# Kernel tuning notes

Measured on AMD Instinct MI355X. Metric: run time of the kernel, lower is better.

The kernel has to match this reference:

```python
import jax, jax.numpy as jnp
import numpy as np
from jax import lax

B, L, H, K = 64, 1024, 768, 4
C1, C2 = 0.1, 0.1


def crf_marginals(feats, maskf, T):
    """Batched linear-chain CRF forward-backward.
    feats: [B,L,K] emission scores, maskf: [B,L] float (1=valid), T: [K,K] transitions.
    Returns marginals [B,L,K] (zeroed at padded positions)."""
    a0 = feats[:, 0]  # [B,K]

    def fwd_step(a, xs):
        f_t, m_t = xs  # [B,K], [B]
        new = f_t + jax.nn.logsumexp(a[:, :, None] + T[None], axis=1)
        a = jnp.where(m_t[:, None] > 0, new, a)  # freeze alpha past last valid token
        return a, a

    _, alphas_rest = lax.scan(fwd_step, a0,
                              (jnp.swapaxes(feats[:, 1:], 0, 1), maskf[:, 1:].T))
    alphas = jnp.concatenate([a0[None], alphas_rest], axis=0)  # [L,B,K]
    logZ = jax.nn.logsumexp(alphas[-1], axis=-1)  # [B] (alpha frozen at last valid t)

    bL = jnp.zeros_like(a0)

    def bwd_step(b, xs):
        f_n, m_n = xs  # emission/mask at t+1
        new = jax.nn.logsumexp(T[None] + (f_n + b)[:, None, :], axis=2)
        b = jnp.where(m_n[:, None] > 0, new, b)  # beta stays 0 until last valid token
        return b, b

    xs = (jnp.swapaxes(feats[:, 1:][:, ::-1], 0, 1), maskf[:, 1:][:, ::-1].T)
    _, betas_rev = lax.scan(bwd_step, bL, xs)
    betas = jnp.concatenate([bL[None], betas_rev], axis=0)[::-1]  # [L,B,K]

    marg = jnp.exp(alphas + betas - logZ[None, :, None]) * maskf.T[:, :, None]
    return jnp.swapaxes(marg, 0, 1)  # [B,L,K]


def _forward(hidden, maskf, w, b, T):
    feats = hidden @ w.T + b                      # [B,L,K] feat2tri
    marg = crf_marginals(feats, maskf, T)
    sp = marg[:, :, 1]                            # select_polarities, masked [B,L]
    gamma = sp.sum(axis=1) / 2.0                  # [B]
    sent_vs = jnp.einsum('bl,blh->bh', sp, hidden) / gamma[:, None]
    s_prob = sp / gamma[:, None]                  # padded-ragged per-token probs
    s_prob_norm = jnp.abs(s_prob).sum(axis=1).mean()
    pena = jax.nn.relu(T[1, 0] - T[0, 0]) + jax.nn.relu(T[0, 1] - T[1, 1])
    norm_pen = C1 * pena + C2 * s_prob_norm
    return sent_vs, norm_pen, s_prob


def setup_inputs():
    key = jax.random.key(0)
    ks = jax.random.split(key, 8)
    hidden = jax.random.normal(ks[0], (B, L, H), dtype=jnp.float32)
    seq_lens = jax.random.randint(ks[1], (B,), L // 4, L + 1)
    # hidden_mask: 0 for valid tokens, nonzero for padding (forward uses mask = hidden_mask==0)
    hidden_mask = (jnp.arange(L)[None, :] >= seq_lens[:, None]).astype(jnp.int32)
    subj_position = jax.random.randint(ks[2], (B, L), -20, 21)
    obj_position = jax.random.randint(ks[3], (B, L), -20, 21)
    pe_inputs = jax.random.randint(ks[4], (B, L), 0, 2 * L)
    pe_binary = jax.random.randint(ks[5], (B, L), 0, 2)
    w_feat2tri = jax.random.normal(ks[6], (K, H), dtype=jnp.float32) * (1.0 / np.sqrt(H)).astype(np.float32)
    b_feat2tri = jnp.zeros((K,), dtype=jnp.float32)
    transitions = jax.random.normal(ks[7], (K, K), dtype=jnp.float32) * 0.1
    return dict(hidden=hidden, hidden_mask=hidden_mask, subj_position=subj_position,
                obj_position=obj_position, seq_lens=seq_lens, pe_inputs=pe_inputs,
                pe_binary=pe_binary, w_feat2tri=w_feat2tri, b_feat2tri=b_feat2tri,
                transitions=transitions)


def reference(hidden, hidden_mask, subj_position, obj_position, seq_lens, pe_inputs,
              pe_binary, w_feat2tri, b_feat2tri, transitions):
    maskf = (hidden_mask == 0).astype(hidden.dtype)
    # relevance is computed in the original forward but never consumed downstream,
    # so it has no effect on outputs; omitted here.
    return _forward(hidden, maskf, w_feat2tri, b_feat2tri, transitions)
```

## Files before the change

### kernel.cpp

```cpp
#include <hip/hip_runtime.h>

#define B 64
#define L 1024
#define H 768
#define NROWS (B * L)
#define LOG2E 1.4426950408889634f
#define CS 16
#define NCH 64
#define NEG -1e30f

#define EXP2(x) __builtin_amdgcn_exp2f(x)
#define LOG2(x) __builtin_amdgcn_logf(x)

__global__ __launch_bounds__(256) void feats_kernel(
    const float* __restrict__ hidden, const float* __restrict__ w,
    const float* __restrict__ bias, float4* __restrict__ featsT)
{
    const int lane = threadIdx.x & 63;
    const int wave = (blockIdx.x * blockDim.x + threadIdx.x) >> 6;
    const int nwaves = (gridDim.x * blockDim.x) >> 6;

    float wr[3][4][4];
#pragma unroll
    for (int c = 0; c < 3; ++c)
#pragma unroll
        for (int j = 0; j < 4; ++j)
#pragma unroll
            for (int k = 0; k < 4; ++k)
                wr[c][j][k] = w[k * H + lane * 4 + 256 * c + j];
    const float bb0 = bias[0], bb1 = bias[1], bb2 = bias[2], bb3 = bias[3];

    for (int row = wave; row < NROWS; row += nwaves) {
        const float4* hrow = reinterpret_cast<const float4*>(hidden) + (size_t)row * (H / 4);
        float acc[4] = {0.f, 0.f, 0.f, 0.f};
#pragma unroll
        for (int c = 0; c < 3; ++c) {
            float4 h = hrow[lane + 64 * c];
            const float hv[4] = {h.x, h.y, h.z, h.w};
#pragma unroll
            for (int j = 0; j < 4; ++j)
#pragma unroll
                for (int k = 0; k < 4; ++k)
                    acc[k] = fmaf(hv[j], wr[c][j][k], acc[k]);
        }
#pragma unroll
        for (int k = 0; k < 4; ++k) {
            float v = acc[k];
#pragma unroll
            for (int s = 32; s >= 1; s >>= 1) v += __shfl_xor(v, s, 64);
            acc[k] = v;
        }
        if (lane == 0) {
            const int b = row >> 10, l = row & 1023;
            featsT[l * B + b] = make_float4((acc[0] + bb0) * LOG2E, (acc[1] + bb1) * LOG2E,
                                            (acc[2] + bb2) * LOG2E, (acc[3] + bb3) * LOG2E);
        }
    }
}

__global__ __launch_bounds__(64) void chunkmat_kernel(
    const float4* __restrict__ featsT, const int* __restrict__ seq_lens,
    const float* __restrict__ T, float* __restrict__ mats)
{
    const int b = threadIdx.x;
    const int dir = blockIdx.x >= NCH;
    const int c = blockIdx.x - (dir ? NCH : 0);
    const int sl = seq_lens[b];
    const int lo = c * CS + 1;
    const int hi = min(c * CS + CS, L - 1);
    const int ns = hi - lo + 1;

    float eT2[4][4];
#pragma unroll
    for (int i = 0; i < 4; ++i)
#pragma unroll
        for (int j = 0; j < 4; ++j) eT2[i][j] = EXP2(T[i * 4 + j] * LOG2E);

    float4 fr[CS];
#pragma unroll
    for (int u = 0; u < CS; ++u) {
        const int t = dir ? max(hi - u, lo) : min(lo + u, hi);
        fr[u] = featsT[t * B + b];
    }

    float M[4][4];
#pragma unroll
    for (int i = 0; i < 4; ++i)
#pragma unroll
        for (int j = 0; j < 4; ++j) M[i][j] = (i == j) ? 0.f : NEG;

    if (dir == 0) {
#pragma unroll
        for (int u = 0; u < CS; ++u) {
            const int t = lo + u;
            const bool valid = (u < ns) && (t < sl);
            const float f[4] = {fr[u].x, fr[u].y, fr[u].z, fr[u].w};
            float nM[4][4];
#pragma unroll
            for (int i = 0; i < 4; ++i) {
                const float rm = fmaxf(fmaxf(M[i][0], M[i][1]), fmaxf(M[i][2], M[i][3]));
                const float e0 = EXP2(M[i][0] - rm), e1 = EXP2(M[i][1] - rm);
                const float e2 = EXP2(M[i][2] - rm), e3 = EXP2(M[i][3] - rm);
#pragma unroll
                for (int j = 0; j < 4; ++j) {
                    const float s = (e0 * eT2[0][j] + e1 * eT2[1][j]) + (e2 * eT2[2][j] + e3 * eT2[3][j]);
                    nM[i][j] = f[j] + rm + LOG2(s);
                }
            }
#pragma unroll
            for (int i = 0; i < 4; ++i)
#pragma unroll
                for (int j = 0; j < 4; ++j) M[i][j] = valid ? nM[i][j] : M[i][j];
        }
    } else {
#pragma unroll
        for (int u = 0; u < CS; ++u) {
            const int n = hi - u;
            const bool valid = (u < ns) && (n < sl);
            const float f[4] = {fr[u].x, fr[u].y, fr[u].z, fr[u].w};
            float nM[4][4];
#pragma unroll
            for (int j = 0; j < 4; ++j) {
                const float c0 = f[0] + M[0][j], c1 = f[1] + M[1][j];
                const float c2 = f[2] + M[2][j], c3 = f[3] + M[3][j];
                const float cm = fmaxf(fmaxf(c0, c1), fmaxf(c2, c3));
                const float g0 = EXP2(c0 - cm), g1 = EXP2(c1 - cm);
                const float g2 = EXP2(c2 - cm), g3 = EXP2(c3 - cm);
#pragma unroll
                for (int i = 0; i < 4; ++i) {
                    const float s = (g0 * eT2[i][0] + g1 * eT2[i][1]) + (g2 * eT2[i][2] + g3 * eT2[i][3]);
                    nM[i][j] = cm + LOG2(s);
                }
            }
#pragma unroll
            for (int i = 0; i < 4; ++i)
#pragma unroll
                for (int j = 0; j < 4; ++j) M[i][j] = valid ? nM[i][j] : M[i][j];
        }
    }
#pragma unroll
    for (int i = 0; i < 4; ++i)
#pragma unroll
        for (int j = 0; j < 4; ++j)
            mats[((dir * NCH + c) * 16 + i * 4 + j) * B + b] = M[i][j];
}

__global__ __launch_bounds__(128) void bound_kernel(
    const float4* __restrict__ featsT, const float* __restrict__ mats,
    float* __restrict__ vbound, float* __restrict__ alpha1,
    float* __restrict__ beta1, float* __restrict__ logZ)
{
    const int b = threadIdx.x & 63;
    const int dir = threadIdx.x >> 6;

    float Ms[4][16];
#pragma unroll
    for (int p = 0; p < 3; ++p) {
        const int cc = dir ? (NCH - 1 - p) : p;
#pragma unroll
        for (int k = 0; k < 16; ++k)
            Ms[p][k] = mats[((dir * NCH + cc) * 16 + k) * B + b];
    }

    float v0, v1, v2, v3;
    if (dir == 0) {
        const float4 f0 = featsT[b];
        v0 = f0.x; v1 = f0.y; v2 = f0.z; v3 = f0.w;
        alpha1[b] = v1;
    } else {
        v0 = v1 = v2 = v3 = 0.f;
        beta1[(L - 1) * B + b] = 0.f;
    }

#pragma unroll
    for (int u = 0; u < NCH; ++u) {
        const int cc = dir ? (NCH - 1 - u) : u;
        vbound[((dir * NCH + cc) * 4 + 0) * B + b] = v0;
        vbound[((dir * NCH + cc) * 4 + 1) * B + b] = v1;
        vbound[((dir * NCH + cc) * 4 + 2) * B + b] = v2;
        vbound[((dir * NCH + cc) * 4 + 3) * B + b] = v3;
        if (u + 3 < NCH) {
            const int cp = dir ? (NCH - 1 - (u + 3)) : (u + 3);
#pragma unroll
            for (int k = 0; k < 16; ++k)
                Ms[(u + 3) & 3][k] = mats[((dir * NCH + cp) * 16 + k) * B + b];
        }
        float n[4];
        if (dir == 0) {
#pragma unroll
            for (int j = 0; j < 4; ++j) {
                const float c0 = v0 + Ms[u & 3][0 * 4 + j], c1 = v1 + Ms[u & 3][1 * 4 + j];
                const float c2 = v2 + Ms[u & 3][2 * 4 + j], c3 = v3 + Ms[u & 3][3 * 4 + j];
                const float m = fmaxf(fmaxf(c0, c1), fmaxf(c2, c3));
                const float s = (EXP2(c0 - m) + EXP2(c1 - m)) + (EXP2(c2 - m) + EXP2(c3 - m));
                n[j] = m + LOG2(s);
            }
        } else {
#pragma unroll
            for (int i = 0; i < 4; ++i) {
                const float c0 = v0 + Ms[u & 3][i * 4 + 0], c1 = v1 + Ms[u & 3][i * 4 + 1];
                const float c2 = v2 + Ms[u & 3][i * 4 + 2], c3 = v3 + Ms[u & 3][i * 4 + 3];
                const float m = fmaxf(fmaxf(c0, c1), fmaxf(c2, c3));
                const float s = (EXP2(c0 - m) + EXP2(c1 - m)) + (EXP2(c2 - m) + EXP2(c3 - m));
                n[i] = m + LOG2(s);
            }
        }
        v0 = n[0]; v1 = n[1]; v2 = n[2]; v3 = n[3];
    }
    if (dir == 0) {
        const float m = fmaxf(fmaxf(v0, v1), fmaxf(v2, v3));
        logZ[b] = m + LOG2(EXP2(v0 - m) + EXP2(v1 - m) + EXP2(v2 - m) + EXP2(v3 - m));
    }
}

__global__ __launch_bounds__(64) void rescan_kernel(
    const float4* __restrict__ featsT, const int* __restrict__ seq_lens,
    const float* __restrict__ T, const float* __restrict__ vbound,
    float* __restrict__ alpha1, float* __restrict__ beta1)
{
    const int b = threadIdx.x;
    const int dir = blockIdx.x >= NCH;
    const int c = blockIdx.x - (dir ? NCH : 0);
    const int sl = seq_lens[b];
    const int lo = c * CS + 1;
    const int hi = min(c * CS + CS, L - 1);
    const int ns = hi - lo + 1;

    float eT2[4][4];
#pragma unroll
    for (int i = 0; i < 4; ++i)
#pragma unroll
        for (int j = 0; j < 4; ++j) eT2[i][j] = EXP2(T[i * 4 + j] * LOG2E);

    float4 fr[CS];
#pragma unroll
    for (int u = 0; u < CS; ++u) {
        const int t = dir ? max(hi - u, lo) : min(lo + u, hi);
        fr[u] = featsT[t * B + b];
    }

    float v0 = vbound[((dir * NCH + c) * 4 + 0) * B + b];
    float v1 = vbound[((dir * NCH + c) * 4 + 1) * B + b];
    float v2 = vbound[((dir * NCH + c) * 4 + 2) * B + b];
    float v3 = vbound[((dir * NCH + c) * 4 + 3) * B + b];

    if (dir == 0) {
#pragma unroll
        for (int u = 0; u < CS; ++u) {
            if (u < ns) {
                const int t = lo + u;
                const bool valid = t < sl;
                const float4 f = fr[u];
                const float m = fmaxf(fmaxf(v0, v1), fmaxf(v2, v3));
                const float e0 = EXP2(v0 - m), e1 = EXP2(v1 - m), e2 = EXP2(v2 - m), e3 = EXP2(v3 - m);
                const float s0 = (e0 * eT2[0][0] + e1 * eT2[1][0]) + (e2 * eT2[2][0] + e3 * eT2[3][0]);
                const float s1 = (e0 * eT2[0][1] + e1 * eT2[1][1]) + (e2 * eT2[2][1] + e3 * eT2[3][1]);
                const float s2 = (e0 * eT2[0][2] + e1 * eT2[1][2]) + (e2 * eT2[2][2] + e3 * eT2[3][2]);
                const float s3 = (e0 * eT2[0][3] + e1 * eT2[1][3]) + (e2 * eT2[2][3] + e3 * eT2[3][3]);
                const float n0 = f.x + m + LOG2(s0), n1 = f.y + m + LOG2(s1);
                const float n2 = f.z + m + LOG2(s2), n3 = f.w + m + LOG2(s3);
                v0 = valid ? n0 : v0; v1 = valid ? n1 : v1;
                v2 = valid ? n2 : v2; v3 = valid ? n3 : v3;
                alpha1[t * B + b] = v1;
            }
        }
    } else {
#pragma unroll
        for (int u = 0; u < CS; ++u) {
            if (u < ns) {
                const int n = hi - u;
                const bool valid = n < sl;
                const float4 f = fr[u];
                const float c0 = f.x + v0, c1 = f.y + v1, c2 = f.z + v2, c3 = f.w + v3;
                const float m = fmaxf(fmaxf(c0, c1), fmaxf(c2, c3));
                const float g0 = EXP2(c0 - m), g1 = EXP2(c1 - m), g2 = EXP2(c2 - m), g3 = EXP2(c3 - m);
                const float s0 = (g0 * eT2[0][0] + g1 * eT2[0][1]) + (g2 * eT2[0][2] + g3 * eT2[0][3]);
                const float s1 = (g0 * eT2[1][0] + g1 * eT2[1][1]) + (g2 * eT2[1][2] + g3 * eT2[1][3]);
                const float s2 = (g0 * eT2[2][0] + g1 * eT2[2][1]) + (g2 * eT2[2][2] + g3 * eT2[2][3]);
                const float s3 = (g0 * eT2[3][0] + g1 * eT2[3][1]) + (g2 * eT2[3][2] + g3 * eT2[3][3]);
                const float n0 = m + LOG2(s0), n1 = m + LOG2(s1);
                const float n2 = m + LOG2(s2), n3 = m + LOG2(s3);
                v0 = valid ? n0 : v0; v1 = valid ? n1 : v1;
                v2 = valid ? n2 : v2; v3 = valid ? n3 : v3;
                beta1[(n - 1) * B + b] = v1;
            }
        }
    }
}

__global__ __launch_bounds__(256) void marg_kernel(
    const float* __restrict__ alpha1, const float* __restrict__ beta1,
    const float* __restrict__ logZ, const int* __restrict__ seq_lens,
    float* __restrict__ normsum, float* __restrict__ sprob)
{
    const int b = blockIdx.x;
    const int tid = threadIdx.x;
    const float lz = logZ[b];
    const int sl = seq_lens[b];
    float v[4];
    float loc = 0.f;
#pragma unroll
    for (int c = 0; c < 4; ++c) {
        const int l = tid + 256 * c;
        const float a1 = alpha1[l * B + b];
        const float be = beta1[l * B + b];
        const float x = (l < sl) ? EXP2(a1 + be - lz) : 0.f;
        v[c] = x;
        loc += x;
    }
#pragma unroll
    for (int s = 32; s >= 1; s >>= 1) loc += __shfl_xor(loc, s, 64);
    __shared__ float red[4];
    if ((tid & 63) == 0) red[tid >> 6] = loc;
    __syncthreads();
    const float tot = red[0] + red[1] + red[2] + red[3];
    const float g = 0.5f * tot;
    const float inv = 1.0f / g;
#pragma unroll
    for (int c = 0; c < 4; ++c)
        sprob[b * L + tid + 256 * c] = v[c] * inv;
    if (tid == 0) normsum[b] = tot * inv;
}

__global__ __launch_bounds__(256) void sentv_kernel(
    const float* __restrict__ hidden, const float* __restrict__ sprob,
    float* __restrict__ partial)
{
    const int b = blockIdx.y;
    const int hc = blockIdx.x % 3;
    const int lc = blockIdx.x / 3;
    const int h = hc * 256 + threadIdx.x;
    const float* hb = hidden + ((size_t)b * L + (size_t)lc * 256) * H + h;
    const float* sp = sprob + b * L + lc * 256;
    float acc = 0.f;
#pragma unroll 8
    for (int l = 0; l < 256; ++l)
        acc = fmaf(sp[l], hb[(size_t)l * H], acc);
    partial[((size_t)lc * B + b) * H + h] = acc;
}

__global__ __launch_bounds__(256) void final_kernel(
    const float* __restrict__ partial, const float* __restrict__ normsum,
    const float* __restrict__ T, float* __restrict__ out)
{
    const int idx = blockIdx.x * 256 + threadIdx.x;
    if (idx < B * H) {
        out[idx] = (partial[idx] + partial[B * H + idx]) +
                   (partial[2 * B * H + idx] + partial[3 * B * H + idx]);
    }
    if (idx == 0) {
        const float pena = fmaxf(T[4] - T[0], 0.f) + fmaxf(T[1] - T[5], 0.f);
        float s = 0.f;
        for (int b2 = 0; b2 < B; ++b2) s += normsum[b2];
        out[B * H] = 0.1f * pena + 0.1f * (s / 64.f);
    }
}

extern "C" void kernel_launch(void* const* d_in, const int* in_sizes, int n_in,
                              void* d_out, int out_size, void* d_ws, size_t ws_size,
                              hipStream_t stream) {
    const float* hidden   = (const float*)d_in[0];
    const int*   seq_lens = (const int*)d_in[4];
    const float* w        = (const float*)d_in[7];
    const float* bias     = (const float*)d_in[8];
    const float* T        = (const float*)d_in[9];

    float* ws = (float*)d_ws;
    float4* featsT  = (float4*)(ws);
    float*  alpha1  = ws + 262144;
    float*  beta1   = ws + 327680;
    float*  logZ    = ws + 393216;
    float*  normsum = ws + 393280;
    float*  partial = ws + 393344;
    float*  mats    = ws + 589952;
    float*  vbound  = ws + 721024;

    float* out   = (float*)d_out;
    float* sprob = out + B * H + 1;

    feats_kernel<<<2048, 256, 0, stream>>>(hidden, w, bias, featsT);
    chunkmat_kernel<<<2 * NCH, 64, 0, stream>>>(featsT, seq_lens, T, mats);
    bound_kernel<<<1, 128, 0, stream>>>(featsT, mats, vbound, alpha1, beta1, logZ);
    rescan_kernel<<<2 * NCH, 64, 0, stream>>>(featsT, seq_lens, T, vbound, alpha1, beta1);
    marg_kernel<<<64, 256, 0, stream>>>(alpha1, beta1, logZ, seq_lens, normsum, sprob);
    sentv_kernel<<<dim3(12, 64), 256, 0, stream>>>(hidden, sprob, partial);
    final_kernel<<<192, 256, 0, stream>>>(partial, normsum, T, out);
}
```

Baseline: 103.8 us.

## Fuse rescan with marginals via shared memory and vectorize sentv over hidden dim

```diff
diff --git a/kernel.cpp b/kernel.cpp
--- a/kernel.cpp
+++ b/kernel.cpp
@@ -58,13 +58,13 @@
     }
 }
 
-__global__ __launch_bounds__(64) void chunkmat_kernel(
+__global__ __launch_bounds__(128) void chunkmat_kernel(
     const float4* __restrict__ featsT, const int* __restrict__ seq_lens,
     const float* __restrict__ T, float* __restrict__ mats)
 {
-    const int b = threadIdx.x;
-    const int dir = blockIdx.x >= NCH;
-    const int c = blockIdx.x - (dir ? NCH : 0);
+    const int b = threadIdx.x & 63;
+    const int dir = threadIdx.x >> 6;
+    const int c = blockIdx.x;
     const int sl = seq_lens[b];
     const int lo = c * CS + 1;
     const int hi = min(c * CS + CS, L - 1);
@@ -147,8 +147,7 @@
 
 __global__ __launch_bounds__(128) void bound_kernel(
     const float4* __restrict__ featsT, const float* __restrict__ mats,
-    float* __restrict__ vbound, float* __restrict__ alpha1,
-    float* __restrict__ beta1, float* __restrict__ logZ)
+    float* __restrict__ vbound, float* __restrict__ logZ)
 {
     const int b = threadIdx.x & 63;
     const int dir = threadIdx.x >> 6;
@@ -166,10 +165,8 @@
     if (dir == 0) {
         const float4 f0 = featsT[b];
         v0 = f0.x; v1 = f0.y; v2 = f0.z; v3 = f0.w;
-        alpha1[b] = v1;
     } else {
         v0 = v1 = v2 = v3 = 0.f;
-        beta1[(L - 1) * B + b] = 0.f;
     }
 
 #pragma unroll
@@ -213,18 +210,18 @@
     }
 }
 
-__global__ __launch_bounds__(64) void rescan_kernel(
+__global__ __launch_bounds__(128) void rescan_sp_kernel(
     const float4* __restrict__ featsT, const int* __restrict__ seq_lens,
     const float* __restrict__ T, const float* __restrict__ vbound,
-    float* __restrict__ alpha1, float* __restrict__ beta1)
-{
-    const int b = threadIdx.x;
-    const int dir = blockIdx.x >= NCH;
-    const int c = blockIdx.x - (dir ? NCH : 0);
+    const float* __restrict__ logZ, float* __restrict__ spu,
+    float* __restrict__ chunksum)
+{
+    const int tid = threadIdx.x;
+    const int b = tid & 63;
+    const int dir = tid >> 6;
+    const int c = blockIdx.x;
     const int sl = seq_lens[b];
-    const int lo = c * CS + 1;
-    const int hi = min(c * CS + CS, L - 1);
-    const int ns = hi - lo + 1;
+    const int base = c * CS;
 
     float eT2[4][4];
 #pragma unroll
@@ -232,43 +229,24 @@
 #pragma unroll
         for (int j = 0; j < 4; ++j) eT2[i][j] = EXP2(T[i * 4 + j] * LOG2E);
 
-    float4 fr[CS];
-#pragma unroll
-    for (int u = 0; u < CS; ++u) {
-        const int t = dir ? max(hi - u, lo) : min(lo + u, hi);
-        fr[u] = featsT[t * B + b];
-    }
-
-    float v0 = vbound[((dir * NCH + c) * 4 + 0) * B + b];
-    float v1 = vbound[((dir * NCH + c) * 4 + 1) * B + b];
-    float v2 = vbound[((dir * NCH + c) * 4 + 2) * B + b];
-    float v3 = vbound[((dir * NCH + c) * 4 + 3) * B + b];
-
-    if (dir == 0) {
+    __shared__ float ldb[CS * 64];
+
+    if (dir == 1) {
+        float v0 = vbound[((NCH + c) * 4 + 0) * B + b];
+        float v1 = vbound[((NCH + c) * 4 + 1) * B + b];
+        float v2 = vbound[((NCH + c) * 4 + 2) * B + b];
+        float v3 = vbound[((NCH + c) * 4 + 3) * B + b];
+        const bool last = (c == NCH - 1);
+        const int hi_n = last ? (L - 1) : (base + CS);
+        const int cnt = last ? (CS - 1) : CS;
+        if (last) ldb[15 * 64 + b] = v1;
+        float4 fr[CS];
+#pragma unroll
+        for (int u = 0; u < CS; ++u) fr[u] = featsT[max(hi_n - u, base + 1) * B + b];
 #pragma unroll
         for (int u = 0; u < CS; ++u) {
-            if (u < ns) {
-                const int t = lo + u;
-                const bool valid = t < sl;
-                const float4 f = fr[u];
-                const float m = fmaxf(fmaxf(v0, v1), fmaxf(v2, v3));
-                const float e0 = EXP2(v0 - m), e1 = EXP2(v1 - m), e2 = EXP2(v2 - m), e3 = EXP2(v3 - m);
-                const float s0 = (e0 * eT2[0][0] + e1 * eT2[1][0]) + (e2 * eT2[2][0] + e3 * eT2[3][0]);
-                const float s1 = (e0 * eT2[0][1] + e1 * eT2[1][1]) + (e2 * eT2[2][1] + e3 * eT2[3][1]);
-                const float s2 = (e0 * eT2[0][2] + e1 * eT2[1][2]) + (e2 * eT2[2][2] + e3 * eT2[3][2]);
-                const float s3 = (e0 * eT2[0][3] + e1 * eT2[1][3]) + (e2 * eT2[2][3] + e3 * eT2[3][3]);
-                const float n0 = f.x + m + LOG2(s0), n1 = f.y + m + LOG2(s1);
-                const float n2 = f.z + m + LOG2(s2), n3 = f.w + m + LOG2(s3);
-                v0 = valid ? n0 : v0; v1 = valid ? n1 : v1;
-                v2 = valid ? n2 : v2; v3 = valid ? n3 : v3;
-                alpha1[t * B + b] = v1;
-            }
-        }
-    } else {
-#pragma unroll
-        for (int u = 0; u < CS; ++u) {
-            if (u < ns) {
-                const int n = hi - u;
+            if (u < cnt) {
+                const int n = hi_n - u;
                 const bool valid = n < sl;
                 const float4 f = fr[u];
                 const float c0 = f.x + v0, c1 = f.y + v1, c2 = f.z + v2, c3 = f.w + v3;
@@ -282,61 +260,123 @@
                 const float n2 = m + LOG2(s2), n3 = m + LOG2(s3);
                 v0 = valid ? n0 : v0; v1 = valid ? n1 : v1;
                 v2 = valid ? n2 : v2; v3 = valid ? n3 : v3;
-                beta1[(n - 1) * B + b] = v1;
+                ldb[(n - 1 - base) * 64 + b] = v1;
             }
         }
     }
-}
-
-__global__ __launch_bounds__(256) void marg_kernel(
-    const float* __restrict__ alpha1, const float* __restrict__ beta1,
-    const float* __restrict__ logZ, const int* __restrict__ seq_lens,
-    float* __restrict__ normsum, float* __restrict__ sprob)
+
+    float av[CS];
+    if (dir == 0) {
+        float a0 = vbound[(c * 4 + 0) * B + b];
+        float a1 = vbound[(c * 4 + 1) * B + b];
+        float a2 = vbound[(c * 4 + 2) * B + b];
+        float a3 = vbound[(c * 4 + 3) * B + b];
+        av[0] = a1;
+        float4 fr[CS - 1];
+#pragma unroll
+        for (int u = 1; u < CS; ++u) fr[u - 1] = featsT[(base + u) * B + b];
+#pragma unroll
+        for (int u = 1; u < CS; ++u) {
+            const int t = base + u;
+            const bool valid = t < sl;
+            const float4 f = fr[u - 1];
+            const float m = fmaxf(fmaxf(a0, a1), fmaxf(a2, a3));
+            const float e0 = EXP2(a0 - m), e1 = EXP2(a1 - m), e2 = EXP2(a2 - m), e3 = EXP2(a3 - m);
+            const float s0 = (e0 * eT2[0][0] + e1 * eT2[1][0]) + (e2 * eT2[2][0] + e3 * eT2[3][0]);
+            const float s1 = (e0 * eT2[0][1] + e1 * eT2[1][1]) + (e2 * eT2[2][1] + e3 * eT2[3][1]);
+            const float s2 = (e0 * eT2[0][2] + e1 * eT2[1][2]) + (e2 * eT2[2][2] + e3 * eT2[3][2]);
+            const float s3 = (e0 * eT2[0][3] + e1 * eT2[1][3]) + (e2 * eT2[2][3] + e3 * eT2[3][3]);
+            const float n0 = f.x + m + LOG2(s0), n1 = f.y + m + LOG2(s1);
+            const float n2 = f.z + m + LOG2(s2), n3 = f.w + m + LOG2(s3);
+            a0 = valid ? n0 : a0; a1 = valid ? n1 : a1;
+            a2 = valid ? n2 : a2; a3 = valid ? n3 : a3;
+            av[u] = a1;
+        }
+    }
+
+    __syncthreads();
+
+    if (dir == 0) {
+        const float lz = logZ[b];
+        float sp[CS];
+        float local = 0.f;
+#pragma unroll
+        for (int u = 0; u < CS; ++u) {
+            const int l = base + u;
+            const float x = (l < sl) ? EXP2(av[u] + ldb[u * 64 + b] - lz) : 0.f;
+            sp[u] = x;
+            local += x;
+        }
+        float4* dst = reinterpret_cast<float4*>(spu + b * L + base);
+#pragma unroll
+        for (int q = 0; q < 4; ++q)
+            dst[q] = make_float4(sp[4 * q], sp[4 * q + 1], sp[4 * q + 2], sp[4 * q + 3]);
+        chunksum[c * 64 + b] = local;
+    }
+}
+
+__global__ __launch_bounds__(192) void sentv_kernel(
+    const float* __restrict__ hidden, const float* __restrict__ spu,
+    const float* __restrict__ chunksum, float* __restrict__ partial)
+{
+    const int lc = blockIdx.x;
+    const int b = blockIdx.y;
+    const int tid = threadIdx.x;
+
+    __shared__ float s_inv;
+    if (tid < 64) {
+        float v = chunksum[tid * 64 + b];
+#pragma unroll
+        for (int s = 32; s >= 1; s >>= 1) v += __shfl_xor(v, s, 64);
+        if (tid == 0) s_inv = 2.0f / v;
+    }
+    __syncthreads();
+    const float inv = s_inv;
+
+    const float4* hb = reinterpret_cast<const float4*>(hidden + ((size_t)b * L + lc * 256) * H) + tid;
+    const float* sp = spu + b * L + lc * 256;
+
+    float4 acc = make_float4(0.f, 0.f, 0.f, 0.f);
+#pragma unroll 4
+    for (int l0 = 0; l0 < 256; l0 += 4) {
+        const float4 s4 = *reinterpret_cast<const float4*>(sp + l0);
+        const float4 h0 = hb[(size_t)(l0 + 0) * 192];
+        const float4 h1 = hb[(size_t)(l0 + 1) * 192];
+        const float4 h2 = hb[(size_t)(l0 + 2) * 192];
+        const float4 h3 = hb[(size_t)(l0 + 3) * 192];
+        acc.x = fmaf(s4.x, h0.x, acc.x); acc.y = fmaf(s4.x, h0.y, acc.y);
+        acc.z = fmaf(s4.x, h0.z, acc.z); acc.w = fmaf(s4.x, h0.w, acc.w);
+        acc.x = fmaf(s4.y, h1.x, acc.x); acc.y = fmaf(s4.y, h1.y, acc.y);
+        acc.z = fmaf(s4.y, h1.z, acc.z); acc.w = fmaf(s4.y, h1.w, acc.w);
+        acc.x = fmaf(s4.z, h2.x, acc.x); acc.y = fmaf(s4.z, h2.y, acc.y);
+        acc.z = fmaf(s4.z, h2.z, acc.z); acc.w = fmaf(s4.z, h2.w, acc.w);
+        acc.x = fmaf(s4.w, h3.x, acc.x); acc.y = fmaf(s4.w, h3.y, acc.y);
+        acc.z = fmaf(s4.w, h3.z, acc.z); acc.w = fmaf(s4.w, h3.w, acc.w);
+    }
+    acc.x *= inv; acc.y *= inv; acc.z *= inv; acc.w *= inv;
+    reinterpret_cast<float4*>(partial)[((size_t)lc * B + b) * 192 + tid] = acc;
+}
+
+__global__ __launch_bounds__(256) void normalize_kernel(
+    const float* __restrict__ spu, const float* __restrict__ chunksum,
+    float* __restrict__ sprob, float* __restrict__ normsum)
 {
     const int b = blockIdx.x;
     const int tid = threadIdx.x;
-    const float lz = logZ[b];
-    const int sl = seq_lens[b];
-    float v[4];
-    float loc = 0.f;
-#pragma unroll
-    for (int c = 0; c < 4; ++c) {
-        const int l = tid + 256 * c;
-        const float a1 = alpha1[l * B + b];
-        const float be = beta1[l * B + b];
-        const float x = (l < sl) ? EXP2(a1 + be - lz) : 0.f;
-        v[c] = x;
-        loc += x;
-    }
-#pragma unroll
-    for (int s = 32; s >= 1; s >>= 1) loc += __shfl_xor(loc, s, 64);
-    __shared__ float red[4];
-    if ((tid & 63) == 0) red[tid >> 6] = loc;
+    __shared__ float s_tot;
+    if (tid < 64) {
+        float v = chunksum[tid * 64 + b];
+#pragma unroll
+        for (int s = 32; s >= 1; s >>= 1) v += __shfl_xor(v, s, 64);
+        if (tid == 0) s_tot = v;
+    }
     __syncthreads();
-    const float tot = red[0] + red[1] + red[2] + red[3];
-    const float g = 0.5f * tot;
-    const float inv = 1.0f / g;
-#pragma unroll
-    for (int c = 0; c < 4; ++c)
-        sprob[b * L + tid + 256 * c] = v[c] * inv;
+    const float tot = s_tot;
+    const float inv = 1.0f / (0.5f * tot);
+    const float4 v4 = reinterpret_cast<const float4*>(spu + b * L)[tid];
+    reinterpret_cast<float4*>(sprob + b * L)[tid] =
+        make_float4(v4.x * inv, v4.y * inv, v4.z * inv, v4.w * inv);
     if (tid == 0) normsum[b] = tot * inv;
-}
-
-__global__ __launch_bounds__(256) void sentv_kernel(
-    const float* __restrict__ hidden, const float* __restrict__ sprob,
-    float* __restrict__ partial)
-{
-    const int b = blockIdx.y;
-    const int hc = blockIdx.x % 3;
-    const int lc = blockIdx.x / 3;
-    const int h = hc * 256 + threadIdx.x;
-    const float* hb = hidden + ((size_t)b * L + (size_t)lc * 256) * H + h;
-    const float* sp = sprob + b * L + lc * 256;
-    float acc = 0.f;
-#pragma unroll 8
-    for (int l = 0; l < 256; ++l)
-        acc = fmaf(sp[l], hb[(size_t)l * H], acc);
-    partial[((size_t)lc * B + b) * H + h] = acc;
 }
 
 __global__ __launch_bounds__(256) void final_kernel(
@@ -366,23 +406,23 @@
     const float* T        = (const float*)d_in[9];
 
     float* ws = (float*)d_ws;
-    float4* featsT  = (float4*)(ws);
-    float*  alpha1  = ws + 262144;
-    float*  beta1   = ws + 327680;
-    float*  logZ    = ws + 393216;
-    float*  normsum = ws + 393280;
-    float*  partial = ws + 393344;
-    float*  mats    = ws + 589952;
-    float*  vbound  = ws + 721024;
+    float4* featsT   = (float4*)(ws);
+    float*  mats     = ws + 262144;
+    float*  vbound   = ws + 393216;
+    float*  logZ     = ws + 425984;
+    float*  chunksum = ws + 426048;
+    float*  spu      = ws + 430144;
+    float*  partial  = ws + 495680;
+    float*  normsum  = ws + 692288;
 
     float* out   = (float*)d_out;
     float* sprob = out + B * H + 1;
 
     feats_kernel<<<2048, 256, 0, stream>>>(hidden, w, bias, featsT);
-    chunkmat_kernel<<<2 * NCH, 64, 0, stream>>>(featsT, seq_lens, T, mats);
-    bound_kernel<<<1, 128, 0, stream>>>(featsT, mats, vbound, alpha1, beta1, logZ);
-    rescan_kernel<<<2 * NCH, 64, 0, stream>>>(featsT, seq_lens, T, vbound, alpha1, beta1);
-    marg_kernel<<<64, 256, 0, stream>>>(alpha1, beta1, logZ, seq_lens, normsum, sprob);
-    sentv_kernel<<<dim3(12, 64), 256, 0, stream>>>(hidden, sprob, partial);
+    chunkmat_kernel<<<NCH, 128, 0, stream>>>(featsT, seq_lens, T, mats);
+    bound_kernel<<<1, 128, 0, stream>>>(featsT, mats, vbound, logZ);
+    rescan_sp_kernel<<<NCH, 128, 0, stream>>>(featsT, seq_lens, T, vbound, logZ, spu, chunksum);
+    sentv_kernel<<<dim3(4, 64), 192, 0, stream>>>(hidden, spu, chunksum, partial);
+    normalize_kernel<<<64, 256, 0, stream>>>(spu, chunksum, sprob, normsum);
     final_kernel<<<192, 256, 0, stream>>>(partial, normsum, T, out);
 }
```

New measurement: 103.5 us. No clear change (-0.3%).
